# Optimization experiments

Hardware: AMD Instinct MI355X
Metric: run time of the kernel (lower is better)

Reference implementation:

```python
import jax, jax.numpy as jnp
import numpy as np

B, N, G = 8, 512, 16          # images, proposals/img, gt boxes/img
C = 91                        # num classes (incl background)
FEAT = 256 * 7 * 7            # pooled RoI feature dim = 12544
REP = 1024                    # TwoMLPHead representation size
FG, BG = 0.5, 0.5             # fg/bg IoU thresholds
BBOX_W = (10.0, 10.0, 5.0, 5.0)
BETA = 1.0 / 9.0              # smooth-L1 beta


def setup_inputs() -> dict:
    key = jax.random.key(0)
    ks = jax.random.split(key, 12)
    # valid xyxy boxes inside an ~800x800 image
    tl = jax.random.uniform(ks[0], (B, N, 2), minval=0.0, maxval=700.0)
    wh = jax.random.uniform(ks[1], (B, N, 2), minval=8.0, maxval=128.0)
    proposals = jnp.concatenate([tl, tl + wh], axis=-1)
    gtl = jax.random.uniform(ks[2], (B, G, 2), minval=0.0, maxval=700.0)
    gwh = jax.random.uniform(ks[3], (B, G, 2), minval=8.0, maxval=128.0)
    gt_boxes = jnp.concatenate([gtl, gtl + gwh], axis=-1)
    gt_labels = jax.random.randint(ks[4], (B, G), 1, C)  # foreground labels 1..C-1
    P = N + G
    features = jax.random.normal(ks[5], (B * P, FEAT), dtype=jnp.float32)
    s = 0.01
    return {
        'proposals': proposals, 'gt_boxes': gt_boxes, 'features': features,
        'W1': jax.random.normal(ks[6], (FEAT, REP), jnp.float32) * s,
        'b1': jnp.zeros((REP,), jnp.float32),
        'W2': jax.random.normal(ks[7], (REP, REP), jnp.float32) * s,
        'b2': jnp.zeros((REP,), jnp.float32),
        'Wcls': jax.random.normal(ks[8], (REP, C), jnp.float32) * s,
        'bcls': jnp.zeros((C,), jnp.float32),
        'Wbox': jax.random.normal(ks[9], (REP, C * 4), jnp.float32) * s,
        'bbox': jnp.zeros((C * 4,), jnp.float32),
        'gt_labels': gt_labels,
    }


def _box_iou(gt, pr):
    # gt: [B,G,4], pr: [B,P,4] -> [B,G,P]
    area_g = (gt[..., 2] - gt[..., 0]) * (gt[..., 3] - gt[..., 1])
    area_p = (pr[..., 2] - pr[..., 0]) * (pr[..., 3] - pr[..., 1])
    lt = jnp.maximum(gt[:, :, None, :2], pr[:, None, :, :2])
    rb = jnp.minimum(gt[:, :, None, 2:], pr[:, None, :, 2:])
    wh = jnp.clip(rb - lt, 0.0)
    inter = wh[..., 0] * wh[..., 1]
    return inter / (area_g[:, :, None] + area_p[:, None, :] - inter)


def _encode(ref, gt):
    # torchvision BoxCoder.encode_single; ref/gt: [...,4]
    wx, wy, ww, wh = BBOX_W
    ew = ref[..., 2] - ref[..., 0]; eh = ref[..., 3] - ref[..., 1]
    ex = ref[..., 0] + 0.5 * ew;    ey = ref[..., 1] + 0.5 * eh
    gw = gt[..., 2] - gt[..., 0];   gh = gt[..., 3] - gt[..., 1]
    gx = gt[..., 0] + 0.5 * gw;     gy = gt[..., 1] + 0.5 * gh
    return jnp.stack([
        wx * (gx - ex) / ew, wy * (gy - ey) / eh,
        ww * jnp.log(gw / ew), wh * jnp.log(gh / eh)], axis=-1)


def reference(proposals, gt_boxes, features, W1, b1, W2, b2, Wcls, bcls, Wbox, bbox, gt_labels):
    # add_gt_proposals
    props = jnp.concatenate([proposals, gt_boxes], axis=1)  # [B,P,4]
    # assign_targets_to_proposals (Matcher, allow_low_quality_matches=False)
    iou = _box_iou(gt_boxes, props)                          # [B,G,P]
    matched_vals = iou.max(axis=1)                           # [B,P]
    matched_idx = iou.argmax(axis=1)                         # [B,P]
    labels = jnp.take_along_axis(gt_labels, matched_idx, axis=1)
    labels = jnp.where(matched_vals < BG, 0, labels)                         # background
    labels = jnp.where((matched_vals >= BG) & (matched_vals < FG), -1, labels)  # ignore
    matched_gt = jnp.take_along_axis(gt_boxes, matched_idx[..., None], axis=1)  # [B,P,4]
    reg_targets = _encode(props, matched_gt).reshape(-1, 4)  # [R,4]
    labels = labels.reshape(-1)                               # [R]

    # TwoMLPHead + FastRCNNPredictor
    x = jax.nn.relu(features @ W1 + b1)
    x = jax.nn.relu(x @ W2 + b2)
    class_logits = x @ Wcls + bcls                            # [R,C]
    box_regression = (x @ Wbox + bbox).reshape(-1, C, 4)      # [R,C,4]

    # fastrcnn_loss (all proposals; ignored labels (-1) masked from CE)
    R = class_logits.shape[0]
    valid = (labels >= 0).astype(class_logits.dtype)
    safe_lab = jnp.clip(labels, 0, C - 1)
    logp = jax.nn.log_softmax(class_logits, axis=-1)
    nll = -jnp.take_along_axis(logp, safe_lab[:, None], axis=1)[:, 0]
    classification_loss = (nll * valid).sum() / jnp.maximum(valid.sum(), 1.0)

    pos = (labels > 0).astype(class_logits.dtype)
    pred = jnp.take_along_axis(box_regression, safe_lab[:, None, None], axis=1)[:, 0]  # [R,4]
    d = jnp.abs(pred - reg_targets)
    sl1 = jnp.where(d < BETA, 0.5 * d * d / BETA, d - 0.5 * BETA).sum(-1)
    box_loss = (sl1 * pos).sum() / R

    return jnp.stack([classification_loss, box_loss])
```

## Files before the change

### kernel.cpp

```cpp
#include <hip/hip_runtime.h>
#include <cstdint>
#include <cstddef>

#define BQ   8
#define NP   512
#define GQ   16
#define PP   528
#define RT   4224
#define CC   91
#define FEATD 12544
#define REPD 1024
#define NH   512
#define NHU  455
#define BETA (1.0f/9.0f)
#define WSC  64.0f

typedef float f32x4 __attribute__((ext_vector_type(4)));

__device__ __forceinline__ unsigned short f2bf(float f) {
  unsigned int x = __float_as_uint(f);
  unsigned int r = (x + 0x7fffu + ((x >> 16) & 1u)) >> 16;
  return (unsigned short)r;
}
__device__ __forceinline__ float bf2f(unsigned short u) {
  return __uint_as_float((unsigned int)u << 16);
}
__device__ __forceinline__ unsigned char f2fp8(float f) {
  return (unsigned char)(__builtin_amdgcn_cvt_pk_fp8_f32(f, 0.0f, 0, false) & 0xff);
}

__device__ __forceinline__ void ld_lds16(const void* g, void* l) {
  __builtin_amdgcn_global_load_lds(
      (const __attribute__((address_space(1))) void*)g,
      (__attribute__((address_space(3))) void*)l, 16, 0, 0);
}

constexpr size_t O_W1T = 0;
constexpr size_t SZ_W1T = (size_t)FEATD * REPD;
constexpr size_t O_W2T = O_W1T + SZ_W1T;
constexpr size_t SZ_W2T = (size_t)REPD * REPD;
constexpr size_t O_WH  = O_W2T + SZ_W2T;
constexpr size_t SZ_WH = (size_t)NH * REPD;
constexpr size_t O_BH  = O_WH + SZ_WH;
constexpr size_t SZ_BH = (size_t)NH * 4;
constexpr size_t O_X1  = O_BH + SZ_BH;
constexpr size_t SZ_X1 = (size_t)RT * REPD;
constexpr size_t O_X2  = O_X1 + SZ_X1;
constexpr size_t O_LAB = O_X2 + SZ_X1;
constexpr size_t O_TGT = O_LAB + (size_t)RT * 4;
constexpr size_t O_NLL = O_TGT + (size_t)RT * 16;
constexpr size_t O_VC  = O_NLL + (size_t)RT * 4;
constexpr size_t O_SL1 = O_VC + (size_t)RT * 4;
constexpr size_t O_PART = ((O_SL1 + (size_t)RT * 4) + 255) & ~(size_t)255;
constexpr size_t SZ_PART = (size_t)4 * RT * REPD * 2;
constexpr size_t O_F8 = O_PART + SZ_PART;

__device__ __forceinline__ void t32(const float* __restrict__ in, unsigned char* __restrict__ out,
                                    int K, int N, int row_off, int out_ld,
                                    int bx, int by, int t, float (*tile)[33]) {
  int tx = t & 31, ty = t >> 5;
  int n0 = bx * 32, k0 = by * 32;
#pragma unroll
  for (int i = 0; i < 4; ++i) {
    int k = k0 + ty + i * 8, n = n0 + tx;
    if (k < K && n < N) tile[ty + i * 8][tx] = in[(size_t)k * N + n];
  }
  __syncthreads();
#pragma unroll
  for (int i = 0; i < 4; ++i) {
    int n = n0 + ty + i * 8, k = k0 + tx;
    if (n < N && k < K) out[(size_t)(n + row_off) * out_ld + k] = f2fp8(tile[tx][ty + i * 8] * WSC);
  }
}

#define NB_CV ((RT * FEATD / 4) / 256)
#define NB_W1 ((REPD/32)*(FEATD/32))
#define NB_W2 ((REPD/32)*(REPD/32))
#define NB_WC (3*(REPD/32))
#define NB_WB (12*(REPD/32))
#define NB_HI 230
#define NB_MT 17
#define NB_PREP (NB_CV+NB_W1+NB_W2+NB_WC+NB_WB+NB_HI+NB_MT)

__global__ void prep(const float* __restrict__ feat, unsigned int* __restrict__ feat8,
                     const float* __restrict__ W1, const float* __restrict__ W2,
                     const float* __restrict__ Wcls, const float* __restrict__ Wbox,
                     const float* __restrict__ bcls, const float* __restrict__ bbox,
                     const float* __restrict__ proposals, const float* __restrict__ gt_boxes,
                     const int* __restrict__ gt_labels,
                     unsigned char* __restrict__ W1t, unsigned char* __restrict__ W2t,
                     unsigned char* __restrict__ Wh, float* __restrict__ bh,
                     int* __restrict__ labels, float* __restrict__ tgts) {
  __shared__ float tile[32][33];
  int b = blockIdx.x, t = threadIdx.x;
  if (b < NB_CV) {
    long i = (long)b * 256 + t;
    float4 f = ((const float4*)feat)[i];
    unsigned int r = (unsigned int)__builtin_amdgcn_cvt_pk_fp8_f32(f.x, f.y, 0, false);
    r = (unsigned int)__builtin_amdgcn_cvt_pk_fp8_f32(f.z, f.w, (int)r, true);
    feat8[i] = r;
    return;
  }
  b -= NB_CV;
  if (b < NB_W1) { t32(W1, W1t, FEATD, REPD, 0, FEATD, b % (REPD/32), b / (REPD/32), t, tile); return; }
  b -= NB_W1;
  if (b < NB_W2) { t32(W2, W2t, REPD, REPD, 0, REPD, b % 32, b / 32, t, tile); return; }
  b -= NB_W2;
  if (b < NB_WC) { t32(Wcls, Wh, REPD, CC, 0, REPD, b % 3, b / 3, t, tile); return; }
  b -= NB_WC;
  if (b < NB_WB) { t32(Wbox, Wh, REPD, 4 * CC, CC, REPD, b % 12, b / 12, t, tile); return; }
  b -= NB_WB;
  if (b < NB_HI) {
    int idx = b * 256 + t;
    const int npad = (NH - NHU) * REPD;
    if (idx < npad) Wh[(size_t)NHU * REPD + idx] = 0;
    else {
      int i2 = idx - npad;
      if (i2 < NH) bh[i2] = (i2 < CC) ? bcls[i2] : (i2 < NHU ? bbox[i2 - CC] : 0.0f);
    }
    return;
  }
  b -= NB_HI;
  int r = b * 256 + t;
  if (r >= RT) return;
  int bi_ = r / PP, p = r % PP;
  float x0, y0, x1, y1;
  if (p < NP) {
    const float* qq = proposals + ((size_t)bi_ * NP + p) * 4;
    x0 = qq[0]; y0 = qq[1]; x1 = qq[2]; y1 = qq[3];
  } else {
    const float* qq = gt_boxes + ((size_t)bi_ * GQ + (p - NP)) * 4;
    x0 = qq[0]; y0 = qq[1]; x1 = qq[2]; y1 = qq[3];
  }
  float ap = (x1 - x0) * (y1 - y0);
  float best = -1.0f; int bg = 0;
#pragma unroll
  for (int g = 0; g < GQ; ++g) {
    const float* gb = gt_boxes + ((size_t)bi_ * GQ + g) * 4;
    float gx0 = gb[0], gy0 = gb[1], gx1 = gb[2], gy1 = gb[3];
    float ag = (gx1 - gx0) * (gy1 - gy0);
    float iw = fmaxf(fminf(gx1, x1) - fmaxf(gx0, x0), 0.0f);
    float ih = fmaxf(fminf(gy1, y1) - fmaxf(gy0, y0), 0.0f);
    float inter = iw * ih;
    float iou = inter / (ag + ap - inter);
    if (iou > best) { best = iou; bg = g; }
  }
  int lab = gt_labels[bi_ * GQ + bg];
  if (best < 0.5f) lab = 0;
  labels[r] = lab;
  const float* gb = gt_boxes + ((size_t)bi_ * GQ + bg) * 4;
  float ew = x1 - x0, eh = y1 - y0;
  float ex = x0 + 0.5f * ew, ey = y0 + 0.5f * eh;
  float gw = gb[2] - gb[0], gh = gb[3] - gb[1];
  float gx = gb[0] + 0.5f * gw, gy = gb[1] + 0.5f * gh;
  tgts[r * 4 + 0] = 10.0f * (gx - ex) / ew;
  tgts[r * 4 + 1] = 10.0f * (gy - ey) / eh;
  tgts[r * 4 + 2] = 5.0f * logf(gw / ew);
  tgts[r * 4 + 3] = 5.0f * logf(gh / eh);
}

__global__ __launch_bounds__(256, 4)
void gemm_f8(const unsigned char* __restrict__ A, const unsigned char* __restrict__ Bt,
             unsigned short* __restrict__ P, int M, int Nc, int K, int Kspl,
             int n_nblk, int n_my, int npairs) {
  __shared__ unsigned char As[128 * 64];
  __shared__ unsigned char Bs[128 * 64];

  const int g = blockIdx.x;
  const int xcd = g & 7;
  const int kix = g >> 3;
  const int n  = kix % n_nblk;
  const int pi = kix / n_nblk;
  const int p  = pi * 8 + xcd;
  if (p >= npairs) return;
  const int y  = p % n_my;
  const int kz = p / n_my;
  const int m0 = y * 128, n0 = n * 128;

  const int tid = threadIdx.x;
  const int w = tid >> 6, L = tid & 63;
  const int q = L >> 4, l16 = L & 15;
  const int wr = (w >> 1) * 64, wc = (w & 1) * 64;
  const size_t kbase = (size_t)kz * Kspl;

  const int lrow = L >> 2;
  const int loff = ((L & 3) ^ ((L >> 3) & 3)) * 16;
  const int sg = 2 * w;
  const unsigned char* gA0 = A  + (size_t)(m0 + sg * 16 + lrow) * K + kbase + loff;
  const unsigned char* gA1 = A  + (size_t)(m0 + (sg + 1) * 16 + lrow) * K + kbase + loff;
  const unsigned char* gB0 = Bt + (size_t)(n0 + sg * 16 + lrow) * K + kbase + loff;
  const unsigned char* gB1 = Bt + (size_t)(n0 + (sg + 1) * 16 + lrow) * K + kbase + loff;
  unsigned char* lA0 = &As[sg * 1024];
  unsigned char* lA1 = &As[(sg + 1) * 1024];
  unsigned char* lB0 = &Bs[sg * 1024];
  unsigned char* lB1 = &Bs[(sg + 1) * 1024];

  const int s2f = (l16 >> 1) & 3;
  const int fo0 = (((q >> 1) ^ s2f) * 16) + (q & 1) * 8;
  const int fo1 = (((2 + (q >> 1)) ^ s2f) * 16) + (q & 1) * 8;
  int ao[4], bo[4];
#pragma unroll
  for (int i = 0; i < 4; ++i) {
    ao[i] = (wr + i * 16 + l16) * 64;
    bo[i] = (wc + i * 16 + l16) * 64;
  }

  f32x4 acc[4][4] = {};
  const int nk = Kspl >> 6;
  for (int kb = 0; kb < nk; ++kb) {
    const int ko = kb * 64;
    ld_lds16(gA0 + ko, lA0);
    ld_lds16(gA1 + ko, lA1);
    ld_lds16(gB0 + ko, lB0);
    ld_lds16(gB1 + ko, lB1);
    __syncthreads();
    long a0[4], a1[4], b0[4], b1[4];
#pragma unroll
    for (int i = 0; i < 4; ++i) {
      a0[i] = *(const long*)&As[ao[i] + fo0];
      a1[i] = *(const long*)&As[ao[i] + fo1];
    }
#pragma unroll
    for (int j = 0; j < 4; ++j) {
      b0[j] = *(const long*)&Bs[bo[j] + fo0];
      b1[j] = *(const long*)&Bs[bo[j] + fo1];
    }
#pragma unroll
    for (int i = 0; i < 4; ++i)
#pragma unroll
      for (int j = 0; j < 4; ++j) {
        acc[i][j] = __builtin_amdgcn_mfma_f32_16x16x32_fp8_fp8(a0[i], b0[j], acc[i][j], 0, 0, 0);
        acc[i][j] = __builtin_amdgcn_mfma_f32_16x16x32_fp8_fp8(a1[i], b1[j], acc[i][j], 0, 0, 0);
      }
    __syncthreads();
  }

  unsigned short* Pz = P + (size_t)kz * M * Nc;
#pragma unroll
  for (int i = 0; i < 4; ++i) {
    int rowb = m0 + wr + i * 16 + q * 4;
#pragma unroll
    for (int j = 0; j < 4; ++j) {
      int col = n0 + wc + j * 16 + l16;
#pragma unroll
      for (int r = 0; r < 4; ++r)
        Pz[(size_t)(rowb + r) * Nc + col] = f2bf(acc[i][j][r]);
    }
  }
}

template <int S>
__global__ void reduce_fp8k(const unsigned short* __restrict__ P, const float* __restrict__ bias,
                            unsigned int* __restrict__ outp, long MN4, int nc4) {
  long i = (long)blockIdx.x * blockDim.x + threadIdx.x;
  long stride = (long)gridDim.x * blockDim.x;
  const ushort4* P4 = (const ushort4*)P;
  const float4* B4 = (const float4*)bias;
  for (; i < MN4; i += stride) {
    float vx = 0, vy = 0, vz = 0, vw = 0;
#pragma unroll
    for (int s = 0; s < S; ++s) {
      ushort4 u = P4[s * MN4 + i];
      vx += bf2f(u.x); vy += bf2f(u.y); vz += bf2f(u.z); vw += bf2f(u.w);
    }
    float4 b = B4[i % nc4];
    vx = fmaxf(vx * (1.0f / WSC) + b.x, 0.0f);
    vy = fmaxf(vy * (1.0f / WSC) + b.y, 0.0f);
    vz = fmaxf(vz * (1.0f / WSC) + b.z, 0.0f);
    vw = fmaxf(vw * (1.0f / WSC) + b.w, 0.0f);
    unsigned int r = (unsigned int)__builtin_amdgcn_cvt_pk_fp8_f32(vx, vy, 0, false);
    r = (unsigned int)__builtin_amdgcn_cvt_pk_fp8_f32(vz, vw, (int)r, true);
    outp[i] = r;
  }
}

__global__ void loss_row(const unsigned short* __restrict__ P, const float* __restrict__ bh,
                         const int* __restrict__ labels, const float* __restrict__ tgts,
                         float* __restrict__ nll_v, float* __restrict__ vc_v,
                         float* __restrict__ sl1_v) {
  int r = blockIdx.x;
  int l = threadIdx.x;
  const size_t SL = (size_t)RT * NH;
  const unsigned short* p0 = P + (size_t)r * NH;
#define COLV(c) ((bf2f(p0[(c)]) + bf2f(p0[SL + (c)]) + bf2f(p0[2 * SL + (c)]) + \
                  bf2f(p0[3 * SL + (c)])) * (1.0f / WSC) + bh[(c)])
  float v1 = COLV(l);
  float v2 = (l < CC - 64) ? COLV(64 + l) : -3.4e38f;
  float m = fmaxf(v1, v2);
#pragma unroll
  for (int o = 32; o; o >>= 1) m = fmaxf(m, __shfl_xor(m, o));
  float e = __expf(v1 - m) + ((l < CC - 64) ? __expf(v2 - m) : 0.0f);
#pragma unroll
  for (int o = 32; o; o >>= 1) e += __shfl_xor(e, o);
  if (l == 0) {
    float lse = m + __logf(e);
    int lab = labels[r];
    int sl = lab < 0 ? 0 : (lab > CC - 1 ? CC - 1 : lab);
    float valid = (lab >= 0) ? 1.0f : 0.0f;
    nll_v[r] = (lse - COLV(sl)) * valid;
    vc_v[r] = valid;
    float s = 0.0f;
#pragma unroll
    for (int d = 0; d < 4; ++d) {
      float pd = COLV(CC + sl * 4 + d);
      float ad = fabsf(pd - tgts[r * 4 + d]);
      s += (ad < BETA) ? 0.5f * ad * ad / BETA : ad - 0.5f * BETA;
    }
    sl1_v[r] = (lab > 0) ? s : 0.0f;
  }
#undef COLV
}

__global__ void reduce_final(const float* __restrict__ nll_v, const float* __restrict__ vc_v,
                             const float* __restrict__ sl1_v, float* __restrict__ out) {
  __shared__ float s1[256], s2[256], s3[256];
  int t = threadIdx.x;
  float a = 0, b = 0, c = 0;
  for (int i = t; i < RT; i += 256) { a += nll_v[i]; b += vc_v[i]; c += sl1_v[i]; }
  s1[t] = a; s2[t] = b; s3[t] = c;
  __syncthreads();
  for (int o = 128; o; o >>= 1) {
    if (t < o) { s1[t] += s1[t + o]; s2[t] += s2[t + o]; s3[t] += s3[t + o]; }
    __syncthreads();
  }
  if (t == 0) {
    out[0] = s1[0] / fmaxf(s2[0], 1.0f);
    out[1] = s3[0] / (float)RT;
  }
}

extern "C" void kernel_launch(void* const* d_in, const int* in_sizes, int n_in,
                              void* d_out, int out_size, void* d_ws, size_t ws_size,
                              hipStream_t stream) {
  const float* proposals = (const float*)d_in[0];
  const float* gt_boxes  = (const float*)d_in[1];
  const float* features  = (const float*)d_in[2];
  const float* W1   = (const float*)d_in[3];
  const float* b1   = (const float*)d_in[4];
  const float* W2   = (const float*)d_in[5];
  const float* b2   = (const float*)d_in[6];
  const float* Wcls = (const float*)d_in[7];
  const float* bcls = (const float*)d_in[8];
  const float* Wbox = (const float*)d_in[9];
  const float* bbox = (const float*)d_in[10];
  const int* gt_labels = (const int*)d_in[11];
  float* out = (float*)d_out;

  char* ws = (char*)d_ws;
  unsigned char* W1t = (unsigned char*)(ws + O_W1T);
  unsigned char* W2t = (unsigned char*)(ws + O_W2T);
  unsigned char* Wh  = (unsigned char*)(ws + O_WH);
  float* bh          = (float*)(ws + O_BH);
  unsigned char* x1  = (unsigned char*)(ws + O_X1);
  unsigned char* x2  = (unsigned char*)(ws + O_X2);
  int* labels        = (int*)(ws + O_LAB);
  float* tgts        = (float*)(ws + O_TGT);
  float* nll_v       = (float*)(ws + O_NLL);
  float* vc_v        = (float*)(ws + O_VC);
  float* sl1_v       = (float*)(ws + O_SL1);
  unsigned short* part = (unsigned short*)(ws + O_PART);
  unsigned char* feat8 = (unsigned char*)(ws + O_F8);

  prep<<<NB_PREP, 256, 0, stream>>>(features, (unsigned int*)feat8, W1, W2, Wcls, Wbox,
                                    bcls, bbox, proposals, gt_boxes, gt_labels,
                                    W1t, W2t, Wh, bh, labels, tgts);

  gemm_f8<<<1088, 256, 0, stream>>>(feat8, W1t, part, RT, REPD, FEATD, FEATD / 4,
                                    8, 33, 132);
  reduce_fp8k<4><<<2048, 256, 0, stream>>>(part, b1, (unsigned int*)x1,
                                           (long)RT * REPD / 4, REPD / 4);

  gemm_f8<<<576, 256, 0, stream>>>(x1, W2t, part, RT, REPD, REPD, REPD / 2,
                                   8, 33, 66);
  reduce_fp8k<2><<<2048, 256, 0, stream>>>(part, b2, (unsigned int*)x2,
                                           (long)RT * REPD / 4, REPD / 4);

  gemm_f8<<<544, 256, 0, stream>>>(x2, Wh, part, RT, NH, REPD, REPD / 4,
                                   4, 33, 132);

  loss_row<<<RT, 64, 0, stream>>>(part, bh, labels, tgts, nll_v, vc_v, sl1_v);
  reduce_final<<<1, 256, 0, stream>>>(nll_v, vc_v, sl1_v, out);
}
```

Measured before the change: 502.5 us.

## Switch FP8 GEMM to 32x32x64 scaled MFMA with new LDS layout

Replaces the 16x16x32 fp8 MFMA tiles (4x4 per wave, two k-steps) with the gfx950 mfma_scale 32x32x64 f8f6f4 instruction (2x2 per wave, one instruction per k-block), using unit scales. The LDS staging layout drops the XOR swizzle and switches to 16-byte chunks per row, so each lane reads two 16-byte vectors instead of several 8-byte loads. This cuts the MFMA instruction count and the LDS read count per k-block, at the cost of possible LDS bank conflicts from the unswizzled layout and a different accumulator-to-row mapping in the epilogue.

```diff
diff --git a/kernel.cpp b/kernel.cpp
--- a/kernel.cpp
+++ b/kernel.cpp
@@ -16,6 +16,8 @@
 #define WSC  64.0f
 
 typedef float f32x4 __attribute__((ext_vector_type(4)));
+typedef int   v8i  __attribute__((ext_vector_type(8)));
+typedef float v16f __attribute__((ext_vector_type(16)));
 
 __device__ __forceinline__ unsigned short f2bf(float f) {
   unsigned int x = __float_as_uint(f);
@@ -179,33 +181,31 @@
 
   const int tid = threadIdx.x;
   const int w = tid >> 6, L = tid & 63;
-  const int q = L >> 4, l16 = L & 15;
+  const int l31 = L & 31, h = L >> 5;
   const int wr = (w >> 1) * 64, wc = (w & 1) * 64;
   const size_t kbase = (size_t)kz * Kspl;
 
-  const int lrow = L >> 2;
-  const int loff = ((L & 3) ^ ((L >> 3) & 3)) * 16;
+  const int srow = L & 15, schk = (L >> 4) * 16;
   const int sg = 2 * w;
-  const unsigned char* gA0 = A  + (size_t)(m0 + sg * 16 + lrow) * K + kbase + loff;
-  const unsigned char* gA1 = A  + (size_t)(m0 + (sg + 1) * 16 + lrow) * K + kbase + loff;
-  const unsigned char* gB0 = Bt + (size_t)(n0 + sg * 16 + lrow) * K + kbase + loff;
-  const unsigned char* gB1 = Bt + (size_t)(n0 + (sg + 1) * 16 + lrow) * K + kbase + loff;
+  const unsigned char* gA0 = A  + (size_t)(m0 + sg * 16 + srow) * K + kbase + schk;
+  const unsigned char* gA1 = A  + (size_t)(m0 + (sg + 1) * 16 + srow) * K + kbase + schk;
+  const unsigned char* gB0 = Bt + (size_t)(n0 + sg * 16 + srow) * K + kbase + schk;
+  const unsigned char* gB1 = Bt + (size_t)(n0 + (sg + 1) * 16 + srow) * K + kbase + schk;
   unsigned char* lA0 = &As[sg * 1024];
   unsigned char* lA1 = &As[(sg + 1) * 1024];
   unsigned char* lB0 = &Bs[sg * 1024];
   unsigned char* lB1 = &Bs[(sg + 1) * 1024];
 
-  const int s2f = (l16 >> 1) & 3;
-  const int fo0 = (((q >> 1) ^ s2f) * 16) + (q & 1) * 8;
-  const int fo1 = (((2 + (q >> 1)) ^ s2f) * 16) + (q & 1) * 8;
-  int ao[4], bo[4];
-#pragma unroll
-  for (int i = 0; i < 4; ++i) {
-    ao[i] = (wr + i * 16 + l16) * 64;
-    bo[i] = (wc + i * 16 + l16) * 64;
-  }
-
-  f32x4 acc[4][4] = {};
+  int ab[2], bb[2];
+#pragma unroll
+  for (int i = 0; i < 2; ++i) {
+    int ra = wr + i * 32 + l31;
+    ab[i] = (ra >> 4) * 1024 + (ra & 15) * 16 + h * 512;
+    int rb = wc + i * 32 + l31;
+    bb[i] = (rb >> 4) * 1024 + (rb & 15) * 16 + h * 512;
+  }
+
+  v16f acc[2][2] = {};
   const int nk = Kspl >> 6;
   for (int kb = 0; kb < nk; ++kb) {
     const int ko = kb * 64;
@@ -214,37 +214,36 @@
     ld_lds16(gB0 + ko, lB0);
     ld_lds16(gB1 + ko, lB1);
     __syncthreads();
-    long a0[4], a1[4], b0[4], b1[4];
-#pragma unroll
-    for (int i = 0; i < 4; ++i) {
-      a0[i] = *(const long*)&As[ao[i] + fo0];
-      a1[i] = *(const long*)&As[ao[i] + fo1];
-    }
-#pragma unroll
-    for (int j = 0; j < 4; ++j) {
-      b0[j] = *(const long*)&Bs[bo[j] + fo0];
-      b1[j] = *(const long*)&Bs[bo[j] + fo1];
-    }
-#pragma unroll
-    for (int i = 0; i < 4; ++i)
-#pragma unroll
-      for (int j = 0; j < 4; ++j) {
-        acc[i][j] = __builtin_amdgcn_mfma_f32_16x16x32_fp8_fp8(a0[i], b0[j], acc[i][j], 0, 0, 0);
-        acc[i][j] = __builtin_amdgcn_mfma_f32_16x16x32_fp8_fp8(a1[i], b1[j], acc[i][j], 0, 0, 0);
+    v8i a[2], b[2];
+#pragma unroll
+    for (int i = 0; i < 2; ++i) {
+      int4 alo = *(const int4*)&As[ab[i]];
+      int4 ahi = *(const int4*)&As[ab[i] + 256];
+      a[i] = (v8i){alo.x, alo.y, alo.z, alo.w, ahi.x, ahi.y, ahi.z, ahi.w};
+      int4 blo = *(const int4*)&Bs[bb[i]];
+      int4 bhi = *(const int4*)&Bs[bb[i] + 256];
+      b[i] = (v8i){blo.x, blo.y, blo.z, blo.w, bhi.x, bhi.y, bhi.z, bhi.w};
+    }
+#pragma unroll
+    for (int i = 0; i < 2; ++i)
+#pragma unroll
+      for (int j = 0; j < 2; ++j)
+        acc[i][j] = __builtin_amdgcn_mfma_scale_f32_32x32x64_f8f6f4(
+            a[i], b[j], acc[i][j], 0, 0, 0, 127, 0, 127);
+    __syncthreads();
+  }
+
+  unsigned short* Pz = P + (size_t)kz * M * Nc;
+#pragma unroll
+  for (int i = 0; i < 2; ++i) {
+#pragma unroll
+    for (int j = 0; j < 2; ++j) {
+      int colb = n0 + wc + j * 32 + l31;
+#pragma unroll
+      for (int r = 0; r < 16; ++r) {
+        int row = m0 + wr + i * 32 + (r & 3) + 8 * (r >> 2) + 4 * h;
+        Pz[(size_t)row * Nc + colb] = f2bf(acc[i][j][r]);
       }
-    __syncthreads();
-  }
-
-  unsigned short* Pz = P + (size_t)kz * M * Nc;
-#pragma unroll
-  for (int i = 0; i < 4; ++i) {
-    int rowb = m0 + wr + i * 16 + q * 4;
-#pragma unroll
-    for (int j = 0; j < 4; ++j) {
-      int col = n0 + wc + j * 16 + l16;
-#pragma unroll
-      for (int r = 0; r < 4; ++r)
-        Pz[(size_t)(rowb + r) * Nc + col] = f2bf(acc[i][j][r]);
     }
   }
 }
```

Result: slower. 523.7 us (+4.2%).
